# Kernel optimization log

Measured on AMD Instinct MI355X. Metric: run time of the kernel, lower is better.

Reference implementation:

```python
import jax, jax.numpy as jnp
import numpy as np

_ALIAS = {11: 11, 13: 11, 16: 11, 21: 21, 22: 21, 23: 21, 31: 31, 32: 31, 33: 31,
          41: 41, 42: 41, 43: 41, 44: 41, 51: 51, 52: 51, 53: 51}
_COMPAT = {11: (11, 13, 16), 21: (14, 15, 21, 22, 23), 31: (15, 31, 32, 33),
           41: (41, 42, 43, 44), 51: (15, 51, 52, 53)}
_VOCAB = 64


def _tables():
    alias = np.full((_VOCAB,), -1, np.int32)
    for k, v in _ALIAS.items():
        alias[k] = v
    compat = np.zeros((_VOCAB, _VOCAB), np.float32)
    has = np.zeros((_VOCAB,), np.bool_)
    for r, toks in _COMPAT.items():
        has[r] = True
        for t in toks:
            compat[r, t] = 1.0
    return jnp.asarray(alias), jnp.asarray(compat), jnp.asarray(has)


def setup_inputs() -> dict:
    key = jax.random.key(0)
    k1, k2, k3, k4 = jax.random.split(key, 4)
    B, T, D, A, S, TTL = 8, 4096, 1024, 32, 16, 64
    H = max(TTL * 4, S * 4)
    hidden = jax.random.normal(k1, (B, T, D), jnp.float32)
    anchor_repr = jax.random.normal(k2, (B, A, D), jnp.float32)
    input_ids = jax.random.randint(k3, (B, T), 0, _VOCAB, jnp.int32)
    # end_idx in [S-1, T-H) so span start >= 0 and full horizon fits in T
    anchor_end = jax.random.randint(k4, (B, A), S - 1, T - H, jnp.int32)
    return {"hidden": hidden, "anchor_repr": anchor_repr, "input_ids": input_ids,
            "anchor_end": anchor_end, "span_len": S, "ttl": TTL}


def reference(hidden, anchor_repr, input_ids, anchor_end, span_len, ttl):
    alias_t, compat_t, has_t = _tables()
    B, T, D = hidden.shape
    A = anchor_end.shape[1]
    S = int(span_len)
    H = max(int(ttl) * 4, S * 4)
    W = H - S + 1
    eps = 1e-8

    bidx = jnp.arange(B)[:, None, None]
    start = anchor_end + 1                                   # [B,A]
    fut_idx = start[..., None] + jnp.arange(H)               # [B,A,H]
    future = hidden[bidx, fut_idx]                           # [B,A,H,D]
    fut_tok = input_ids[bidx, fut_idx]                       # [B,A,H]
    span_idx = (anchor_end - S + 1)[..., None] + jnp.arange(S)
    span = input_ids[bidx, span_idx]                         # [B,A,S]
    anchor_tok = input_ids[jnp.arange(B)[:, None], anchor_end]  # [B,A]

    # hidden-space stats (cosine_similarity with F.cosine_similarity eps)
    mean_future = future.mean(axis=2)                        # [B,A,D]
    nr = jnp.maximum(jnp.linalg.norm(anchor_repr, axis=-1), eps)
    nf = jnp.maximum(jnp.linalg.norm(mean_future, axis=-1), eps)
    sim = (anchor_repr * mean_future).sum(-1) / (nr * nf)    # [B,A]
    future_shift = jnp.linalg.norm(future - anchor_repr[:, :, None, :], axis=-1).mean(-1)
    hidden_c = jnp.maximum(0.0, (1.0 - sim) / 2.0)
    token_c = 1.0 - (fut_tok == anchor_tok[..., None]).astype(jnp.float32).mean(-1)

    # sliding windows over the horizon
    win_idx = jnp.arange(W)[:, None] + jnp.arange(S)[None, :]  # [W,S]
    win = fut_tok[:, :, win_idx]                               # [B,A,W,S]
    eq = (win == span[:, :, None, :]).astype(jnp.float32)     # [B,A,W,S]
    exact = eq.mean(-1)                                       # [B,A,W]
    pos_w = jnp.linspace(1.0, 0.4, S)
    pos_w = pos_w / pos_w.sum()
    positional = (eq * pos_w).sum(-1)

    # set-overlap: count distinct anchor tokens present in window
    eqmat = span[..., :, None] == span[..., None, :]          # [B,A,S,S]
    tri = jnp.tril(jnp.ones((S, S), bool), -1)
    first_occ = ~(eqmat & tri).any(-1)                        # first occurrence mask
    first_f = first_occ.astype(jnp.float32)
    denom = first_f.sum(-1)                                   # |set(anchor_span)|
    in_win = (win[..., :, None] == span[:, :, None, None, :]).any(-2)  # [B,A,W,S]
    overlap = (in_win.astype(jnp.float32) * first_f[:, :, None, :]).sum(-1) / denom[:, :, None]

    # infer_reference_root: first aliased token, else mode (smallest on ties)
    alias_span = alias_t[span]                                # [B,A,S], -1 if no alias
    has_a = alias_span >= 0
    first_i = jnp.argmax(has_a, -1)
    first_root = jnp.take_along_axis(alias_span, first_i[..., None], -1)[..., 0]
    counts = eqmat.sum(-1)
    maxc = counts.max(-1, keepdims=True)
    mode = jnp.where(counts == maxc, span, _VOCAB).min(-1)
    root = jnp.where(has_a.any(-1), first_root, mode)         # [B,A]

    r4 = root[:, :, None, None]
    root_pers = (win == r4).astype(jnp.float32).mean(-1)      # [B,A,W]
    alias_c = (alias_t[win] == r4).astype(jnp.float32).mean(-1)
    hard = compat_t[r4, win].mean(-1)
    regime = jnp.where(has_t[root][:, :, None],
                       0.55 * hard + 0.2 * overlap + 0.15 * alias_c + 0.1 * root_pers,
                       0.45 * exact + 0.3 * overlap + 0.1 * alias_c + 0.15 * root_pers)

    sims = 0.25 * exact + 0.15 * overlap + 0.35 * positional + 0.25 * regime
    best = sims.max(-1)
    mrp = root_pers.mean(-1)
    mrc = regime.mean(-1)
    dmass = (sims >= 0.6).astype(jnp.float32).mean(-1)
    dcoh = 0.6 * sims.mean(-1) + 0.25 * mrp + 0.15 * mrc
    pattern_c = 1.0 - (0.6 * best + 0.2 * mrp + 0.2 * mrc)

    contr = jnp.clip(0.2 * hidden_c + 0.2 * token_c + 0.6 * pattern_c, 0.0, 1.0)
    # [8,B,A]: contradiction, future_shift, similarity, hidden_c, token_c, pattern_c, mass, coherence
    return jnp.stack([contr, future_shift, sim, hidden_c, token_c, pattern_c, dmass, dcoh], 0)
```

## Files before the change

kernel.cpp:

```cpp
#include <hip/hip_runtime.h>
#include <math.h>

constexpr int kB = 8;
constexpr int kT = 4096;
constexpr int kD = 1024;
constexpr int kA = 32;
constexpr int kS = 16;
constexpr int kH = 256;
constexpr int kW = kH - kS + 1;
constexpr int NC = kD / 256;

constexpr int SPLIT = 8;
constexpr int RPS   = kH / SPLIT;
constexpr int NT1   = 256;
constexpr int NW1   = NT1 / 64;
constexpr int NWG1  = kB * kA * SPLIT;
constexpr int NT2   = 256;
constexpr int NW2   = NT2 / 64;

constexpr int NTF = 512;
constexpr int NWF = NTF / 64;

__device__ inline float wredsum(float v) {
#pragma unroll
    for (int m = 32; m >= 1; m >>= 1) v += __shfl_xor(v, m, 64);
    return v;
}
__device__ inline float wredmax(float v) {
#pragma unroll
    for (int m = 32; m >= 1; m >>= 1) v = fmaxf(v, __shfl_xor(v, m, 64));
    return v;
}

__device__ inline int alias_of(int t) {
    switch (t) {
        case 11: case 13: case 16: return 11;
        case 21: case 22: case 23: return 21;
        case 31: case 32: case 33: return 31;
        case 41: case 42: case 43: case 44: return 41;
        case 51: case 52: case 53: return 51;
        default: return -1;
    }
}

__global__ __launch_bounds__(NT1, 4) void phaseA_kernel(
    const float* __restrict__ hidden,
    const float* __restrict__ anchor_repr,
    const int*   __restrict__ anchor_end,
    float*       __restrict__ partial,
    float*       __restrict__ pshift)
{
    __shared__ float smean[NW1][kD];
    __shared__ float swshift[NW1];

    const int id = blockIdx.x;
    const int lb = (id & 7) * (NWG1 / 8) + (id >> 3);
    const int ba    = lb / SPLIT;
    const int slice = lb % SPLIT;
    const int b     = ba / kA;
    const int tid  = threadIdx.x;
    const int lane = tid & 63;
    const int wave = tid >> 6;

    const int e     = anchor_end[ba];
    const int start = e + 1;

    const float* arow = anchor_repr + (size_t)ba * kD;
    float4 anc[NC];
#pragma unroll
    for (int c = 0; c < NC; ++c) anc[c] = *(const float4*)(arow + 256 * c + 4 * lane);

    const float* hbase =
        hidden + ((size_t)b * kT + start + slice * RPS) * kD + 4 * lane;

    float sum[NC][4];
#pragma unroll
    for (int c = 0; c < NC; ++c)
#pragma unroll
        for (int j = 0; j < 4; ++j) sum[c][j] = 0.f;

    float shift_acc = 0.f;
    for (int hh = 0; hh < RPS; hh += 2 * NW1) {
        const float* r0 = hbase + (size_t)(hh + wave) * kD;
        const float* r1 = hbase + (size_t)(hh + wave + NW1) * kD;
        float ss0 = 0.f, ss1 = 0.f;
#pragma unroll
        for (int c = 0; c < NC; ++c) {
            float4 x0 = *(const float4*)(r0 + 256 * c);
            float4 x1 = *(const float4*)(r1 + 256 * c);
            float4 a  = anc[c];
            sum[c][0] += x0.x + x1.x;
            sum[c][1] += x0.y + x1.y;
            sum[c][2] += x0.z + x1.z;
            sum[c][3] += x0.w + x1.w;
            float d0 = x0.x - a.x, d1 = x0.y - a.y, d2 = x0.z - a.z, d3 = x0.w - a.w;
            float g0 = x1.x - a.x, g1 = x1.y - a.y, g2 = x1.z - a.z, g3 = x1.w - a.w;
            ss0 += d0*d0 + d1*d1 + d2*d2 + d3*d3;
            ss1 += g0*g0 + g1*g1 + g2*g2 + g3*g3;
        }
        ss0 = wredsum(ss0);
        ss1 = wredsum(ss1);
        shift_acc += sqrtf(ss0) + sqrtf(ss1);
    }
#pragma unroll
    for (int c = 0; c < NC; ++c)
        *(float4*)&smean[wave][256 * c + 4 * lane] =
            make_float4(sum[c][0], sum[c][1], sum[c][2], sum[c][3]);
    if (lane == 0) swshift[wave] = shift_acc;
    __syncthreads();

    float4 t = make_float4(0.f, 0.f, 0.f, 0.f);
#pragma unroll
    for (int w = 0; w < NW1; ++w) {
        const float4 p = *(const float4*)&smean[w][4 * tid];
        t.x += p.x; t.y += p.y; t.z += p.z; t.w += p.w;
    }
    *(float4*)(partial + ((size_t)lb << 10) + 4 * tid) = t;
    if (tid == 0) {
        float s = 0.f;
#pragma unroll
        for (int w = 0; w < NW1; ++w) s += swshift[w];
        pshift[lb] = s;
    }
}

__global__ __launch_bounds__(NT2, 1) void phaseB_kernel(
    const float* __restrict__ anchor_repr,
    const int*   __restrict__ input_ids,
    const int*   __restrict__ anchor_end,
    const float* __restrict__ partial,
    const float* __restrict__ pshift,
    float*       __restrict__ out)
{
    __shared__ int   sfut[kH];
    __shared__ int   sspan[kS];
    __shared__ float sposw[kS];
    __shared__ float sr1[NW2], sr2[NW2], sr3[NW2], sr4[NW2], sr5[NW2];
    __shared__ float s_sim, s_shift, s_hidc, s_tokc;
    __shared__ int   s_root, s_has;
    __shared__ unsigned long long s_spanmask, s_amask, s_hmask;
    __shared__ float s_denom;

    const int ba   = blockIdx.x;
    const int b    = ba / kA;
    const int tid  = threadIdx.x;
    const int lane = tid & 63;
    const int wave = tid >> 6;

    const int e     = anchor_end[ba];
    const int start = e + 1;
    const int* ids  = input_ids + b * kT;
    const int anchor_tok = ids[e];

    sfut[tid] = ids[start + tid];
    if (tid < kS) {
        sspan[tid] = ids[e - kS + 1 + tid];
        sposw[tid] = (1.0f - 0.04f * (float)tid) * (1.0f / 11.2f);
    }

    const float* arow = anchor_repr + (size_t)ba * kD;
    float4 acc = make_float4(0.f, 0.f, 0.f, 0.f);
#pragma unroll
    for (int s = 0; s < SPLIT; ++s) {
        const float4 p =
            *(const float4*)(partial + (((size_t)ba * SPLIT + s) << 10) + 4 * tid);
        acc.x += p.x; acc.y += p.y; acc.z += p.z; acc.w += p.w;
    }
    const float4 av = *(const float4*)(arow + 4 * tid);
    const float inv_h = 1.0f / (float)kH;
    float mx = acc.x * inv_h, my = acc.y * inv_h, mz = acc.z * inv_h, mw = acc.w * inv_h;
    float pm2  = mx*mx + my*my + mz*mz + mw*mw;
    float pdot = mx*av.x + my*av.y + mz*av.z + mw*av.w;
    float pa2  = av.x*av.x + av.y*av.y + av.z*av.z + av.w*av.w;
    float peq  = (sfut[tid] == anchor_tok) ? 1.f : 0.f;
    pm2 = wredsum(pm2); pdot = wredsum(pdot); pa2 = wredsum(pa2); peq = wredsum(peq);
    if (lane == 0) { sr1[wave] = pm2; sr2[wave] = pdot; sr3[wave] = pa2; sr4[wave] = peq; }
    __syncthreads();

    if (tid == 0) {
        float m2 = 0.f, dt = 0.f, a2 = 0.f, eqc = 0.f;
        for (int w = 0; w < NW2; ++w) { m2 += sr1[w]; dt += sr2[w]; a2 += sr3[w]; eqc += sr4[w]; }
        float shift = 0.f;
        for (int s = 0; s < SPLIT; ++s) shift += pshift[ba * SPLIT + s];
        float nf = fmaxf(sqrtf(m2), 1e-8f);
        float nr = fmaxf(sqrtf(a2), 1e-8f);
        float sim = dt / (nr * nf);
        s_sim   = sim;
        s_shift = shift * (1.0f / kH);
        s_hidc  = fmaxf(0.f, (1.f - sim) * 0.5f);
        s_tokc  = 1.f - eqc * (1.0f / kH);
    }
    if (tid == 64) {
        unsigned long long spanmask = 0;
        for (int s = 0; s < kS; ++s) spanmask |= 1ull << sspan[s];
        int root = -1;
        for (int s = 0; s < kS; ++s) { int al = alias_of(sspan[s]); if (al >= 0) { root = al; break; } }
        if (root < 0) {
            int counts[kS], maxc = 0;
            for (int s = 0; s < kS; ++s) {
                int c = 0;
                for (int s2 = 0; s2 < kS; ++s2) c += (sspan[s2] == sspan[s]) ? 1 : 0;
                counts[s] = c; if (c > maxc) maxc = c;
            }
            int mode = 64;
            for (int s = 0; s < kS; ++s) if (counts[s] == maxc && sspan[s] < mode) mode = sspan[s];
            root = mode;
        }
        unsigned long long am = 0, hm = 0; int has = 0;
        switch (root) {
            case 11: am = (1ull<<11)|(1ull<<13)|(1ull<<16);            hm = am;                       has = 1; break;
            case 21: am = (1ull<<21)|(1ull<<22)|(1ull<<23);            hm = am|(1ull<<14)|(1ull<<15); has = 1; break;
            case 31: am = (1ull<<31)|(1ull<<32)|(1ull<<33);            hm = am|(1ull<<15);            has = 1; break;
            case 41: am = (1ull<<41)|(1ull<<42)|(1ull<<43)|(1ull<<44); hm = am;                       has = 1; break;
            case 51: am = (1ull<<51)|(1ull<<52)|(1ull<<53);            hm = am|(1ull<<15);            has = 1; break;
            default: break;
        }
        s_root = root; s_has = has; s_spanmask = spanmask; s_amask = am; s_hmask = hm;
        s_denom = (float)__popcll(spanmask);
    }
    __syncthreads();

    const int root = s_root, has = s_has;
    const unsigned long long spanmask = s_spanmask, amask = s_amask, hmask = s_hmask;
    const float inv_denom = 1.0f / s_denom;

    float sims = -1e30f, rootpers = 0.f, regime = 0.f, simsum = 0.f, cnt = 0.f;
    if (tid < kW) {
        float wex = 0.f, wpos = 0.f, wrp = 0.f, wal = 0.f, whard = 0.f;
        unsigned long long wm = 0;
#pragma unroll
        for (int s = 0; s < kS; ++s) {
            int tok = sfut[tid + s];
            wm |= 1ull << tok;
            bool eq = (tok == sspan[s]);
            wex  += eq ? 1.f : 0.f;
            wpos += eq ? sposw[s] : 0.f;
            wrp  += (tok == root) ? 1.f : 0.f;
            wal  += ((amask >> tok) & 1ull) ? 1.f : 0.f;
            whard += ((hmask >> tok) & 1ull) ? 1.f : 0.f;
        }
        float exact  = wex * (1.f / kS);
        float overlap = (float)__popcll(wm & spanmask) * inv_denom;
        rootpers = wrp * (1.f / kS);
        float aliasc = wal * (1.f / kS);
        float hard   = whard * (1.f / kS);
        regime = has ? (0.55f*hard  + 0.2f*overlap + 0.15f*aliasc + 0.1f*rootpers)
                     : (0.45f*exact + 0.3f*overlap + 0.1f*aliasc  + 0.15f*rootpers);
        sims = 0.25f*exact + 0.15f*overlap + 0.35f*wpos + 0.25f*regime;
        simsum = sims;
        cnt = (sims >= 0.6f) ? 1.f : 0.f;
    }
    float rmax = wredmax(sims);
    float rsum = wredsum(simsum);
    float rrp  = wredsum(rootpers);
    float rreg = wredsum(regime);
    float rcnt = wredsum(cnt);
    if (lane == 0) { sr1[wave] = rmax; sr2[wave] = rsum; sr3[wave] = rrp; sr4[wave] = rreg; sr5[wave] = rcnt; }
    __syncthreads();

    if (tid == 0) {
        float best = -1e30f, ssum = 0.f, srp = 0.f, sreg = 0.f, scnt = 0.f;
        for (int w = 0; w < NW2; ++w) {
            best = fmaxf(best, sr1[w]); ssum += sr2[w]; srp += sr3[w]; sreg += sr4[w]; scnt += sr5[w];
        }
        const float invW = 1.0f / (float)kW;
        float msims = ssum * invW, mrp = srp * invW, mrc = sreg * invW, dmass = scnt * invW;
        float dcoh      = 0.6f*msims + 0.25f*mrp + 0.15f*mrc;
        float pattern_c = 1.f - (0.6f*best + 0.2f*mrp + 0.2f*mrc);
        float contr     = 0.2f*s_hidc + 0.2f*s_tokc + 0.6f*pattern_c;
        contr = fminf(fmaxf(contr, 0.f), 1.f);
        const int n = kB * kA;
        out[0*n + ba] = contr;
        out[1*n + ba] = s_shift;
        out[2*n + ba] = s_sim;
        out[3*n + ba] = s_hidc;
        out[4*n + ba] = s_tokc;
        out[5*n + ba] = pattern_c;
        out[6*n + ba] = dmass;
        out[7*n + ba] = dcoh;
    }
}

__global__ __launch_bounds__(NTF, 1) void monitor_kernel(
    const float* __restrict__ hidden,
    const float* __restrict__ anchor_repr,
    const int*   __restrict__ input_ids,
    const int*   __restrict__ anchor_end,
    float*       __restrict__ out)
{
    __shared__ float smean[NWF][kD];
    __shared__ int   sfut[kH];
    __shared__ int   sspan[kS];
    __shared__ float sposw[kS];
    __shared__ float sr1[NWF], sr2[NWF], sr3[NWF], sr4[NWF], sr5[NWF];
    __shared__ float s_sim, s_shift, s_hidc, s_tokc;
    __shared__ int   s_root, s_has;
    __shared__ unsigned long long s_spanmask, s_amask, s_hmask;
    __shared__ float s_denom;

    const int ba   = blockIdx.x;
    const int b    = ba / kA;
    const int tid  = threadIdx.x;
    const int lane = tid & 63;
    const int wave = tid >> 6;

    const int e     = anchor_end[ba];
    const int start = e + 1;
    const int* ids  = input_ids + b * kT;
    const int anchor_tok = ids[e];

    if (tid < kH) sfut[tid] = ids[start + tid];
    if (tid < kS) {
        sspan[tid] = ids[e - kS + 1 + tid];
        sposw[tid] = (1.0f - 0.04f * (float)tid) * (1.0f / 11.2f);
    }

    const float* arow = anchor_repr + (size_t)ba * kD;
    float4 anc[NC];
#pragma unroll
    for (int c = 0; c < NC; ++c) anc[c] = *(const float4*)(arow + 256 * c + 4 * lane);
    const float* hbase = hidden + ((size_t)b * kT + start) * kD + 4 * lane;

    float sum[NC][4];
#pragma unroll
    for (int c = 0; c < NC; ++c)
#pragma unroll
        for (int j = 0; j < 4; ++j) sum[c][j] = 0.f;

    float shift_acc = 0.f;
    for (int h = wave; h < kH; h += 2 * NWF) {
        const float* r0 = hbase + (size_t)h * kD;
        const float* r1 = hbase + (size_t)(h + NWF) * kD;
        float ss0 = 0.f, ss1 = 0.f;
#pragma unroll
        for (int c = 0; c < NC; ++c) {
            float4 x0 = *(const float4*)(r0 + 256 * c);
            float4 x1 = *(const float4*)(r1 + 256 * c);
            float4 a  = anc[c];
            sum[c][0] += x0.x + x1.x;
            sum[c][1] += x0.y + x1.y;
            sum[c][2] += x0.z + x1.z;
            sum[c][3] += x0.w + x1.w;
            float d0 = x0.x - a.x, d1 = x0.y - a.y, d2 = x0.z - a.z, d3 = x0.w - a.w;
            float g0 = x1.x - a.x, g1 = x1.y - a.y, g2 = x1.z - a.z, g3 = x1.w - a.w;
            ss0 += d0*d0 + d1*d1 + d2*d2 + d3*d3;
            ss1 += g0*g0 + g1*g1 + g2*g2 + g3*g3;
        }
        ss0 = wredsum(ss0);
        ss1 = wredsum(ss1);
        shift_acc += sqrtf(ss0) + sqrtf(ss1);
    }
#pragma unroll
    for (int c = 0; c < NC; ++c)
#pragma unroll
        for (int j = 0; j < 4; ++j) smean[wave][256 * c + 4 * lane + j] = sum[c][j];
    if (lane == 0) sr1[wave] = shift_acc;
    __syncthreads();

    float pm2 = 0.f, pdot = 0.f, pa2 = 0.f;
#pragma unroll
    for (int j = 0; j < kD / NTF; ++j) {
        int d = tid * (kD / NTF) + j;
        float tot = 0.f;
#pragma unroll
        for (int w2 = 0; w2 < NWF; ++w2) tot += smean[w2][d];
        float m  = tot * (1.0f / kH);
        float av = arow[d];
        pm2 += m * m; pdot += m * av; pa2 += av * av;
    }
    float peq = (tid < kH && sfut[tid] == anchor_tok) ? 1.f : 0.f;
    pm2 = wredsum(pm2); pdot = wredsum(pdot); pa2 = wredsum(pa2); peq = wredsum(peq);
    if (lane == 0) { sr2[wave] = pm2; sr3[wave] = pdot; sr4[wave] = pa2; sr5[wave] = peq; }
    __syncthreads();

    if (tid == 0) {
        float shift = 0.f, m2 = 0.f, dt = 0.f, a2 = 0.f, eqc = 0.f;
        for (int w2 = 0; w2 < NWF; ++w2) {
            shift += sr1[w2]; m2 += sr2[w2]; dt += sr3[w2]; a2 += sr4[w2]; eqc += sr5[w2];
        }
        float nf = fmaxf(sqrtf(m2), 1e-8f);
        float nr = fmaxf(sqrtf(a2), 1e-8f);
        float sim = dt / (nr * nf);
        s_sim   = sim;
        s_shift = shift * (1.0f / kH);
        s_hidc  = fmaxf(0.f, (1.f - sim) * 0.5f);
        s_tokc  = 1.f - eqc * (1.0f / kH);
    }
    if (tid == 64) {
        unsigned long long spanmask = 0;
        for (int s = 0; s < kS; ++s) spanmask |= 1ull << sspan[s];
        int root = -1;
        for (int s = 0; s < kS; ++s) { int al = alias_of(sspan[s]); if (al >= 0) { root = al; break; } }
        if (root < 0) {
            int counts[kS], maxc = 0;
            for (int s = 0; s < kS; ++s) {
                int c = 0;
                for (int s2 = 0; s2 < kS; ++s2) c += (sspan[s2] == sspan[s]) ? 1 : 0;
                counts[s] = c; if (c > maxc) maxc = c;
            }
            int mode = 64;
            for (int s = 0; s < kS; ++s) if (counts[s] == maxc && sspan[s] < mode) mode = sspan[s];
            root = mode;
        }
        unsigned long long am = 0, hm = 0; int has = 0;
        switch (root) {
            case 11: am = (1ull<<11)|(1ull<<13)|(1ull<<16);            hm = am;                       has = 1; break;
            case 21: am = (1ull<<21)|(1ull<<22)|(1ull<<23);            hm = am|(1ull<<14)|(1ull<<15); has = 1; break;
            case 31: am = (1ull<<31)|(1ull<<32)|(1ull<<33);            hm = am|(1ull<<15);            has = 1; break;
            case 41: am = (1ull<<41)|(1ull<<42)|(1ull<<43)|(1ull<<44); hm = am;                       has = 1; break;
            case 51: am = (1ull<<51)|(1ull<<52)|(1ull<<53);            hm = am|(1ull<<15);            has = 1; break;
            default: break;
        }
        s_root = root; s_has = has; s_spanmask = spanmask; s_amask = am; s_hmask = hm;
        s_denom = (float)__popcll(spanmask);
    }
    __syncthreads();

    const int root = s_root, has = s_has;
    const unsigned long long spanmask = s_spanmask, amask = s_amask, hmask = s_hmask;
    const float inv_denom = 1.0f / s_denom;

    float sims = -1e30f, rootpers = 0.f, regime = 0.f, simsum = 0.f, cnt = 0.f;
    if (tid < kW) {
        float wex = 0.f, wpos = 0.f, wrp = 0.f, wal = 0.f, whard = 0.f;
        unsigned long long wm = 0;
#pragma unroll
        for (int s = 0; s < kS; ++s) {
            int tok = sfut[tid + s];
            wm |= 1ull << tok;
            bool eq = (tok == sspan[s]);
            wex  += eq ? 1.f : 0.f;
            wpos += eq ? sposw[s] : 0.f;
            wrp  += (tok == root) ? 1.f : 0.f;
            wal  += ((amask >> tok) & 1ull) ? 1.f : 0.f;
            whard += ((hmask >> tok) & 1ull) ? 1.f : 0.f;
        }
        float exact  = wex * (1.f / kS);
        float overlap = (float)__popcll(wm & spanmask) * inv_denom;
        rootpers = wrp * (1.f / kS);
        float aliasc = wal * (1.f / kS);
        float hard   = whard * (1.f / kS);
        regime = has ? (0.55f*hard  + 0.2f*overlap + 0.15f*aliasc + 0.1f*rootpers)
                     : (0.45f*exact + 0.3f*overlap + 0.1f*aliasc  + 0.15f*rootpers);
        sims = 0.25f*exact + 0.15f*overlap + 0.35f*wpos + 0.25f*regime;
        simsum = sims;
        cnt = (sims >= 0.6f) ? 1.f : 0.f;
    }
    float rmax = wredmax(sims);
    float rsum = wredsum(simsum);
    float rrp  = wredsum(rootpers);
    float rreg = wredsum(regime);
    float rcnt = wredsum(cnt);
    if (lane == 0) { sr1[wave] = rmax; sr2[wave] = rsum; sr3[wave] = rrp; sr4[wave] = rreg; sr5[wave] = rcnt; }
    __syncthreads();

    if (tid == 0) {
        float best = -1e30f, ssum = 0.f, srp = 0.f, sreg = 0.f, scnt = 0.f;
        for (int w2 = 0; w2 < NWF; ++w2) {
            best = fmaxf(best, sr1[w2]); ssum += sr2[w2]; srp += sr3[w2]; sreg += sr4[w2]; scnt += sr5[w2];
        }
        const float invW = 1.0f / (float)kW;
        float msims = ssum * invW, mrp = srp * invW, mrc = sreg * invW, dmass = scnt * invW;
        float dcoh      = 0.6f*msims + 0.25f*mrp + 0.15f*mrc;
        float pattern_c = 1.f - (0.6f*best + 0.2f*mrp + 0.2f*mrc);
        float contr     = 0.2f*s_hidc + 0.2f*s_tokc + 0.6f*pattern_c;
        contr = fminf(fmaxf(contr, 0.f), 1.f);
        const int n = kB * kA;
        out[0*n + ba] = contr;
        out[1*n + ba] = s_shift;
        out[2*n + ba] = s_sim;
        out[3*n + ba] = s_hidc;
        out[4*n + ba] = s_tokc;
        out[5*n + ba] = pattern_c;
        out[6*n + ba] = dmass;
        out[7*n + ba] = dcoh;
    }
}

extern "C" void kernel_launch(void* const* d_in, const int* in_sizes, int n_in,
                              void* d_out, int out_size, void* d_ws, size_t ws_size,
                              hipStream_t stream) {
    const float* hidden      = (const float*)d_in[0];
    const float* anchor_repr = (const float*)d_in[1];
    const int*   input_ids   = (const int*)d_in[2];
    const int*   anchor_end  = (const int*)d_in[3];
    float* out = (float*)d_out;

    const size_t n_partial = (size_t)NWG1 * kD;
    const size_t need      = (n_partial + NWG1) * sizeof(float);

    if (d_ws != nullptr && ws_size >= need) {
        float* partial = (float*)d_ws;
        float* pshift  = partial + n_partial;
        hipLaunchKernelGGL(phaseA_kernel, dim3(NWG1), dim3(NT1), 0, stream,
                           hidden, anchor_repr, anchor_end, partial, pshift);
        hipLaunchKernelGGL(phaseB_kernel, dim3(kB * kA), dim3(NT2), 0, stream,
                           anchor_repr, input_ids, anchor_end, partial, pshift, out);
    } else {
        hipLaunchKernelGGL(monitor_kernel, dim3(kB * kA), dim3(NTF), 0, stream,
                           hidden, anchor_repr, input_ids, anchor_end, out);
    }
}
```

Before: 215.1 us.

## Fuse two-phase split reduction into single 1024-thread kernel per anchor

Replaces the two-kernel scheme (256×8 split partial-sum blocks plus a combine kernel) with one fused kernel: one 1024-thread block per anchor that streams all 256 future rows, reduces in shared memory, and computes the token metrics. This removes the partial-sum workspace traffic and the second launch. Each wave now handles four rows per step with batched shuffle reductions to raise memory-level parallelism. In exchange the grid shrinks to 256 blocks, which may underfill the GPU and limit bandwidth compared with 2048 split blocks.

Result: no change. 212.6 us (-1.2%).

```diff
diff --git a/kernel.cpp b/kernel.cpp
--- a/kernel.cpp
+++ b/kernel.cpp
@@ -10,16 +10,10 @@
 constexpr int kW = kH - kS + 1;
 constexpr int NC = kD / 256;
 
-constexpr int SPLIT = 8;
-constexpr int RPS   = kH / SPLIT;
-constexpr int NT1   = 256;
-constexpr int NW1   = NT1 / 64;
-constexpr int NWG1  = kB * kA * SPLIT;
-constexpr int NT2   = 256;
-constexpr int NW2   = NT2 / 64;
-
-constexpr int NTF = 512;
-constexpr int NWF = NTF / 64;
+constexpr int NT = 1024;
+constexpr int NW = NT / 64;
+constexpr int RPW = kH / NW;
+constexpr int GRP = 4;
 
 __device__ inline float wredsum(float v) {
 #pragma unroll
@@ -43,106 +37,27 @@
     }
 }
 
-__global__ __launch_bounds__(NT1, 4) void phaseA_kernel(
+__global__ __launch_bounds__(NT) void monitor_kernel(
     const float* __restrict__ hidden,
-    const float* __restrict__ anchor_repr,
-    const int*   __restrict__ anchor_end,
-    float*       __restrict__ partial,
-    float*       __restrict__ pshift)
-{
-    __shared__ float smean[NW1][kD];
-    __shared__ float swshift[NW1];
-
-    const int id = blockIdx.x;
-    const int lb = (id & 7) * (NWG1 / 8) + (id >> 3);
-    const int ba    = lb / SPLIT;
-    const int slice = lb % SPLIT;
-    const int b     = ba / kA;
-    const int tid  = threadIdx.x;
-    const int lane = tid & 63;
-    const int wave = tid >> 6;
-
-    const int e     = anchor_end[ba];
-    const int start = e + 1;
-
-    const float* arow = anchor_repr + (size_t)ba * kD;
-    float4 anc[NC];
-#pragma unroll
-    for (int c = 0; c < NC; ++c) anc[c] = *(const float4*)(arow + 256 * c + 4 * lane);
-
-    const float* hbase =
-        hidden + ((size_t)b * kT + start + slice * RPS) * kD + 4 * lane;
-
-    float sum[NC][4];
-#pragma unroll
-    for (int c = 0; c < NC; ++c)
-#pragma unroll
-        for (int j = 0; j < 4; ++j) sum[c][j] = 0.f;
-
-    float shift_acc = 0.f;
-    for (int hh = 0; hh < RPS; hh += 2 * NW1) {
-        const float* r0 = hbase + (size_t)(hh + wave) * kD;
-        const float* r1 = hbase + (size_t)(hh + wave + NW1) * kD;
-        float ss0 = 0.f, ss1 = 0.f;
-#pragma unroll
-        for (int c = 0; c < NC; ++c) {
-            float4 x0 = *(const float4*)(r0 + 256 * c);
-            float4 x1 = *(const float4*)(r1 + 256 * c);
-            float4 a  = anc[c];
-            sum[c][0] += x0.x + x1.x;
-            sum[c][1] += x0.y + x1.y;
-            sum[c][2] += x0.z + x1.z;
-            sum[c][3] += x0.w + x1.w;
-            float d0 = x0.x - a.x, d1 = x0.y - a.y, d2 = x0.z - a.z, d3 = x0.w - a.w;
-            float g0 = x1.x - a.x, g1 = x1.y - a.y, g2 = x1.z - a.z, g3 = x1.w - a.w;
-            ss0 += d0*d0 + d1*d1 + d2*d2 + d3*d3;
-            ss1 += g0*g0 + g1*g1 + g2*g2 + g3*g3;
-        }
-        ss0 = wredsum(ss0);
-        ss1 = wredsum(ss1);
-        shift_acc += sqrtf(ss0) + sqrtf(ss1);
-    }
-#pragma unroll
-    for (int c = 0; c < NC; ++c)
-        *(float4*)&smean[wave][256 * c + 4 * lane] =
-            make_float4(sum[c][0], sum[c][1], sum[c][2], sum[c][3]);
-    if (lane == 0) swshift[wave] = shift_acc;
-    __syncthreads();
-
-    float4 t = make_float4(0.f, 0.f, 0.f, 0.f);
-#pragma unroll
-    for (int w = 0; w < NW1; ++w) {
-        const float4 p = *(const float4*)&smean[w][4 * tid];
-        t.x += p.x; t.y += p.y; t.z += p.z; t.w += p.w;
-    }
-    *(float4*)(partial + ((size_t)lb << 10) + 4 * tid) = t;
-    if (tid == 0) {
-        float s = 0.f;
-#pragma unroll
-        for (int w = 0; w < NW1; ++w) s += swshift[w];
-        pshift[lb] = s;
-    }
-}
-
-__global__ __launch_bounds__(NT2, 1) void phaseB_kernel(
     const float* __restrict__ anchor_repr,
     const int*   __restrict__ input_ids,
     const int*   __restrict__ anchor_end,
-    const float* __restrict__ partial,
-    const float* __restrict__ pshift,
     float*       __restrict__ out)
 {
+    __shared__ float smean[NW][kD];
     __shared__ int   sfut[kH];
     __shared__ int   sspan[kS];
     __shared__ float sposw[kS];
-    __shared__ float sr1[NW2], sr2[NW2], sr3[NW2], sr4[NW2], sr5[NW2];
+    __shared__ float sr1[NW], sr2[NW], sr3[NW], sr4[NW], sr5[NW];
     __shared__ float s_sim, s_shift, s_hidc, s_tokc;
     __shared__ int   s_root, s_has;
     __shared__ unsigned long long s_spanmask, s_amask, s_hmask;
     __shared__ float s_denom;
 
-    const int ba   = blockIdx.x;
-    const int b    = ba / kA;
+    const int id = blockIdx.x;
+    const int ba = (id & 7) * 32 + (id >> 3);
+    const int b  = ba / kA;
+
     const int tid  = threadIdx.x;
     const int lane = tid & 63;
     const int wave = tid >> 6;
@@ -152,36 +67,74 @@
     const int* ids  = input_ids + b * kT;
     const int anchor_tok = ids[e];
 
-    sfut[tid] = ids[start + tid];
+    if (tid < kH) sfut[tid] = ids[start + tid];
     if (tid < kS) {
         sspan[tid] = ids[e - kS + 1 + tid];
         sposw[tid] = (1.0f - 0.04f * (float)tid) * (1.0f / 11.2f);
     }
 
     const float* arow = anchor_repr + (size_t)ba * kD;
-    float4 acc = make_float4(0.f, 0.f, 0.f, 0.f);
-#pragma unroll
-    for (int s = 0; s < SPLIT; ++s) {
-        const float4 p =
-            *(const float4*)(partial + (((size_t)ba * SPLIT + s) << 10) + 4 * tid);
-        acc.x += p.x; acc.y += p.y; acc.z += p.z; acc.w += p.w;
-    }
-    const float4 av = *(const float4*)(arow + 4 * tid);
-    const float inv_h = 1.0f / (float)kH;
-    float mx = acc.x * inv_h, my = acc.y * inv_h, mz = acc.z * inv_h, mw = acc.w * inv_h;
-    float pm2  = mx*mx + my*my + mz*mz + mw*mw;
-    float pdot = mx*av.x + my*av.y + mz*av.z + mw*av.w;
-    float pa2  = av.x*av.x + av.y*av.y + av.z*av.z + av.w*av.w;
-    float peq  = (sfut[tid] == anchor_tok) ? 1.f : 0.f;
+    float4 anc[NC];
+#pragma unroll
+    for (int c = 0; c < NC; ++c) anc[c] = *(const float4*)(arow + 256 * c + 4 * lane);
+    const float* hbase = hidden + ((size_t)b * kT + start) * kD + 4 * lane;
+
+    float sum[NC][4];
+#pragma unroll
+    for (int c = 0; c < NC; ++c)
+#pragma unroll
+        for (int j = 0; j < 4; ++j) sum[c][j] = 0.f;
+
+    float shift_acc = 0.f;
+    for (int g = 0; g < RPW / GRP; ++g) {
+        float ss[GRP];
+#pragma unroll
+        for (int k = 0; k < GRP; ++k) ss[k] = 0.f;
+#pragma unroll
+        for (int k = 0; k < GRP; ++k) {
+            const float* rp = hbase + (size_t)(wave + NW * (g * GRP + k)) * kD;
+#pragma unroll
+            for (int c = 0; c < NC; ++c) {
+                float4 x = *(const float4*)(rp + 256 * c);
+                float4 a = anc[c];
+                sum[c][0] += x.x; sum[c][1] += x.y; sum[c][2] += x.z; sum[c][3] += x.w;
+                float d0 = x.x - a.x, d1 = x.y - a.y, d2 = x.z - a.z, d3 = x.w - a.w;
+                ss[k] += d0*d0 + d1*d1 + d2*d2 + d3*d3;
+            }
+        }
+#pragma unroll
+        for (int m = 32; m >= 1; m >>= 1) {
+#pragma unroll
+            for (int k = 0; k < GRP; ++k) ss[k] += __shfl_xor(ss[k], m, 64);
+        }
+#pragma unroll
+        for (int k = 0; k < GRP; ++k) shift_acc += sqrtf(ss[k]);
+    }
+#pragma unroll
+    for (int c = 0; c < NC; ++c)
+        *(float4*)&smean[wave][256 * c + 4 * lane] =
+            make_float4(sum[c][0], sum[c][1], sum[c][2], sum[c][3]);
+    if (lane == 0) sr1[wave] = shift_acc;
+    __syncthreads();
+
+    float tot = 0.f;
+#pragma unroll
+    for (int w = 0; w < NW; ++w) tot += smean[w][tid];
+    float m  = tot * (1.0f / kH);
+    float av = arow[tid];
+    float pm2  = m * m;
+    float pdot = m * av;
+    float pa2  = av * av;
+    float peq  = (tid < kH && sfut[tid] == anchor_tok) ? 1.f : 0.f;
     pm2 = wredsum(pm2); pdot = wredsum(pdot); pa2 = wredsum(pa2); peq = wredsum(peq);
-    if (lane == 0) { sr1[wave] = pm2; sr2[wave] = pdot; sr3[wave] = pa2; sr4[wave] = peq; }
+    if (lane == 0) { sr2[wave] = pm2; sr3[wave] = pdot; sr4[wave] = pa2; sr5[wave] = peq; }
     __syncthreads();
 
     if (tid == 0) {
-        float m2 = 0.f, dt = 0.f, a2 = 0.f, eqc = 0.f;
-        for (int w = 0; w < NW2; ++w) { m2 += sr1[w]; dt += sr2[w]; a2 += sr3[w]; eqc += sr4[w]; }
-        float shift = 0.f;
-        for (int s = 0; s < SPLIT; ++s) shift += pshift[ba * SPLIT + s];
+        float shift = 0.f, m2 = 0.f, dt = 0.f, a2 = 0.f, eqc = 0.f;
+        for (int w = 0; w < NW; ++w) {
+            shift += sr1[w]; m2 += sr2[w]; dt += sr3[w]; a2 += sr4[w]; eqc += sr5[w];
+        }
         float nf = fmaxf(sqrtf(m2), 1e-8f);
         float nr = fmaxf(sqrtf(a2), 1e-8f);
         float sim = dt / (nr * nf);
@@ -260,7 +213,7 @@
 
     if (tid == 0) {
         float best = -1e30f, ssum = 0.f, srp = 0.f, sreg = 0.f, scnt = 0.f;
-        for (int w = 0; w < NW2; ++w) {
+        for (int w = 0; w < NW; ++w) {
             best = fmaxf(best, sr1[w]); ssum += sr2[w]; srp += sr3[w]; sreg += sr4[w]; scnt += sr5[w];
         }
         const float invW = 1.0f / (float)kW;
@@ -281,202 +234,6 @@
     }
 }
 
-__global__ __launch_bounds__(NTF, 1) void monitor_kernel(
-    const float* __restrict__ hidden,
-    const float* __restrict__ anchor_repr,
-    const int*   __restrict__ input_ids,
-    const int*   __restrict__ anchor_end,
-    float*       __restrict__ out)
-{
-    __shared__ float smean[NWF][kD];
-    __shared__ int   sfut[kH];
-    __shared__ int   sspan[kS];
-    __shared__ float sposw[kS];
-    __shared__ float sr1[NWF], sr2[NWF], sr3[NWF], sr4[NWF], sr5[NWF];
-    __shared__ float s_sim, s_shift, s_hidc, s_tokc;
-    __shared__ int   s_root, s_has;
-    __shared__ unsigned long long s_spanmask, s_amask, s_hmask;
-    __shared__ float s_denom;
-
-    const int ba   = blockIdx.x;
-    const int b    = ba / kA;
-    const int tid  = threadIdx.x;
-    const int lane = tid & 63;
-    const int wave = tid >> 6;
-
-    const int e     = anchor_end[ba];
-    const int start = e + 1;
-    const int* ids  = input_ids + b * kT;
-    const int anchor_tok = ids[e];
-
-    if (tid < kH) sfut[tid] = ids[start + tid];
-    if (tid < kS) {
-        sspan[tid] = ids[e - kS + 1 + tid];
-        sposw[tid] = (1.0f - 0.04f * (float)tid) * (1.0f / 11.2f);
-    }
-
-    const float* arow = anchor_repr + (size_t)ba * kD;
-    float4 anc[NC];
-#pragma unroll
-    for (int c = 0; c < NC; ++c) anc[c] = *(const float4*)(arow + 256 * c + 4 * lane);
-    const float* hbase = hidden + ((size_t)b * kT + start) * kD + 4 * lane;
-
-    float sum[NC][4];
-#pragma unroll
-    for (int c = 0; c < NC; ++c)
-#pragma unroll
-        for (int j = 0; j < 4; ++j) sum[c][j] = 0.f;
-
-    float shift_acc = 0.f;
-    for (int h = wave; h < kH; h += 2 * NWF) {
-        const float* r0 = hbase + (size_t)h * kD;
-        const float* r1 = hbase + (size_t)(h + NWF) * kD;
-        float ss0 = 0.f, ss1 = 0.f;
-#pragma unroll
-        for (int c = 0; c < NC; ++c) {
-            float4 x0 = *(const float4*)(r0 + 256 * c);
-            float4 x1 = *(const float4*)(r1 + 256 * c);
-            float4 a  = anc[c];
-            sum[c][0] += x0.x + x1.x;
-            sum[c][1] += x0.y + x1.y;
-            sum[c][2] += x0.z + x1.z;
-            sum[c][3] += x0.w + x1.w;
-            float d0 = x0.x - a.x, d1 = x0.y - a.y, d2 = x0.z - a.z, d3 = x0.w - a.w;
-            float g0 = x1.x - a.x, g1 = x1.y - a.y, g2 = x1.z - a.z, g3 = x1.w - a.w;
-            ss0 += d0*d0 + d1*d1 + d2*d2 + d3*d3;
-            ss1 += g0*g0 + g1*g1 + g2*g2 + g3*g3;
-        }
-        ss0 = wredsum(ss0);
-        ss1 = wredsum(ss1);
-        shift_acc += sqrtf(ss0) + sqrtf(ss1);
-    }
-#pragma unroll
-    for (int c = 0; c < NC; ++c)
-#pragma unroll
-        for (int j = 0; j < 4; ++j) smean[wave][256 * c + 4 * lane + j] = sum[c][j];
-    if (lane == 0) sr1[wave] = shift_acc;
-    __syncthreads();
-
-    float pm2 = 0.f, pdot = 0.f, pa2 = 0.f;
-#pragma unroll
-    for (int j = 0; j < kD / NTF; ++j) {
-        int d = tid * (kD / NTF) + j;
-        float tot = 0.f;
-#pragma unroll
-        for (int w2 = 0; w2 < NWF; ++w2) tot += smean[w2][d];
-        float m  = tot * (1.0f / kH);
-        float av = arow[d];
-        pm2 += m * m; pdot += m * av; pa2 += av * av;
-    }
-    float peq = (tid < kH && sfut[tid] == anchor_tok) ? 1.f : 0.f;
-    pm2 = wredsum(pm2); pdot = wredsum(pdot); pa2 = wredsum(pa2); peq = wredsum(peq);
-    if (lane == 0) { sr2[wave] = pm2; sr3[wave] = pdot; sr4[wave] = pa2; sr5[wave] = peq; }
-    __syncthreads();
-
-    if (tid == 0) {
-        float shift = 0.f, m2 = 0.f, dt = 0.f, a2 = 0.f, eqc = 0.f;
-        for (int w2 = 0; w2 < NWF; ++w2) {
-            shift += sr1[w2]; m2 += sr2[w2]; dt += sr3[w2]; a2 += sr4[w2]; eqc += sr5[w2];
-        }
-        float nf = fmaxf(sqrtf(m2), 1e-8f);
-        float nr = fmaxf(sqrtf(a2), 1e-8f);
-        float sim = dt / (nr * nf);
-        s_sim   = sim;
-        s_shift = shift * (1.0f / kH);
-        s_hidc  = fmaxf(0.f, (1.f - sim) * 0.5f);
-        s_tokc  = 1.f - eqc * (1.0f / kH);
-    }
-    if (tid == 64) {
-        unsigned long long spanmask = 0;
-        for (int s = 0; s < kS; ++s) spanmask |= 1ull << sspan[s];
-        int root = -1;
-        for (int s = 0; s < kS; ++s) { int al = alias_of(sspan[s]); if (al >= 0) { root = al; break; } }
-        if (root < 0) {
-            int counts[kS], maxc = 0;
-            for (int s = 0; s < kS; ++s) {
-                int c = 0;
-                for (int s2 = 0; s2 < kS; ++s2) c += (sspan[s2] == sspan[s]) ? 1 : 0;
-                counts[s] = c; if (c > maxc) maxc = c;
-            }
-            int mode = 64;
-            for (int s = 0; s < kS; ++s) if (counts[s] == maxc && sspan[s] < mode) mode = sspan[s];
-            root = mode;
-        }
-        unsigned long long am = 0, hm = 0; int has = 0;
-        switch (root) {
-            case 11: am = (1ull<<11)|(1ull<<13)|(1ull<<16);            hm = am;                       has = 1; break;
-            case 21: am = (1ull<<21)|(1ull<<22)|(1ull<<23);            hm = am|(1ull<<14)|(1ull<<15); has = 1; break;
-            case 31: am = (1ull<<31)|(1ull<<32)|(1ull<<33);            hm = am|(1ull<<15);            has = 1; break;
-            case 41: am = (1ull<<41)|(1ull<<42)|(1ull<<43)|(1ull<<44); hm = am;                       has = 1; break;
-            case 51: am = (1ull<<51)|(1ull<<52)|(1ull<<53);            hm = am|(1ull<<15);            has = 1; break;
-            default: break;
-        }
-        s_root = root; s_has = has; s_spanmask = spanmask; s_amask = am; s_hmask = hm;
-        s_denom = (float)__popcll(spanmask);
-    }
-    __syncthreads();
-
-    const int root = s_root, has = s_has;
-    const unsigned long long spanmask = s_spanmask, amask = s_amask, hmask = s_hmask;
-    const float inv_denom = 1.0f / s_denom;
-
-    float sims = -1e30f, rootpers = 0.f, regime = 0.f, simsum = 0.f, cnt = 0.f;
-    if (tid < kW) {
-        float wex = 0.f, wpos = 0.f, wrp = 0.f, wal = 0.f, whard = 0.f;
-        unsigned long long wm = 0;
-#pragma unroll
-        for (int s = 0; s < kS; ++s) {
-            int tok = sfut[tid + s];
-            wm |= 1ull << tok;
-            bool eq = (tok == sspan[s]);
-            wex  += eq ? 1.f : 0.f;
-            wpos += eq ? sposw[s] : 0.f;
-            wrp  += (tok == root) ? 1.f : 0.f;
-            wal  += ((amask >> tok) & 1ull) ? 1.f : 0.f;
-            whard += ((hmask >> tok) & 1ull) ? 1.f : 0.f;
-        }
-        float exact  = wex * (1.f / kS);
-        float overlap = (float)__popcll(wm & spanmask) * inv_denom;
-        rootpers = wrp * (1.f / kS);
-        float aliasc = wal * (1.f / kS);
-        float hard   = whard * (1.f / kS);
-        regime = has ? (0.55f*hard  + 0.2f*overlap + 0.15f*aliasc + 0.1f*rootpers)
-                     : (0.45f*exact + 0.3f*overlap + 0.1f*aliasc  + 0.15f*rootpers);
-        sims = 0.25f*exact + 0.15f*overlap + 0.35f*wpos + 0.25f*regime;
-        simsum = sims;
-        cnt = (sims >= 0.6f) ? 1.f : 0.f;
-    }
-    float rmax = wredmax(sims);
-    float rsum = wredsum(simsum);
-    float rrp  = wredsum(rootpers);
-    float rreg = wredsum(regime);
-    float rcnt = wredsum(cnt);
-    if (lane == 0) { sr1[wave] = rmax; sr2[wave] = rsum; sr3[wave] = rrp; sr4[wave] = rreg; sr5[wave] = rcnt; }
-    __syncthreads();
-
-    if (tid == 0) {
-        float best = -1e30f, ssum = 0.f, srp = 0.f, sreg = 0.f, scnt = 0.f;
-        for (int w2 = 0; w2 < NWF; ++w2) {
-            best = fmaxf(best, sr1[w2]); ssum += sr2[w2]; srp += sr3[w2]; sreg += sr4[w2]; scnt += sr5[w2];
-        }
-        const float invW = 1.0f / (float)kW;
-        float msims = ssum * invW, mrp = srp * invW, mrc = sreg * invW, dmass = scnt * invW;
-        float dcoh      = 0.6f*msims + 0.25f*mrp + 0.15f*mrc;
-        float pattern_c = 1.f - (0.6f*best + 0.2f*mrp + 0.2f*mrc);
-        float contr     = 0.2f*s_hidc + 0.2f*s_tokc + 0.6f*pattern_c;
-        contr = fminf(fmaxf(contr, 0.f), 1.f);
-        const int n = kB * kA;
-        out[0*n + ba] = contr;
-        out[1*n + ba] = s_shift;
-        out[2*n + ba] = s_sim;
-        out[3*n + ba] = s_hidc;
-        out[4*n + ba] = s_tokc;
-        out[5*n + ba] = pattern_c;
-        out[6*n + ba] = dmass;
-        out[7*n + ba] = dcoh;
-    }
-}
-
 extern "C" void kernel_launch(void* const* d_in, const int* in_sizes, int n_in,
                               void* d_out, int out_size, void* d_ws, size_t ws_size,
                               hipStream_t stream) {
@@ -485,19 +242,8 @@
     const int*   input_ids   = (const int*)d_in[2];
     const int*   anchor_end  = (const int*)d_in[3];
     float* out = (float*)d_out;
-
-    const size_t n_partial = (size_t)NWG1 * kD;
-    const size_t need      = (n_partial + NWG1) * sizeof(float);
-
-    if (d_ws != nullptr && ws_size >= need) {
-        float* partial = (float*)d_ws;
-        float* pshift  = partial + n_partial;
-        hipLaunchKernelGGL(phaseA_kernel, dim3(NWG1), dim3(NT1), 0, stream,
-                           hidden, anchor_repr, anchor_end, partial, pshift);
-        hipLaunchKernelGGL(phaseB_kernel, dim3(kB * kA), dim3(NT2), 0, stream,
-                           anchor_repr, input_ids, anchor_end, partial, pshift, out);
-    } else {
-        hipLaunchKernelGGL(monitor_kernel, dim3(kB * kA), dim3(NTF), 0, stream,
-                           hidden, anchor_repr, input_ids, anchor_end, out);
-    }
-}
+    (void)d_ws; (void)ws_size;
+
+    hipLaunchKernelGGL(monitor_kernel, dim3(kB * kA), dim3(NT), 0, stream,
+                       hidden, anchor_repr, input_ids, anchor_end, out);
+}
```
